# Kernel tuning notes

Measured on AMD Instinct MI355X. Metric: run time of the kernel, lower is better.

## Reference

```python
import jax, jax.numpy as jnp
import numpy as np

L, N, E = 2048, 2, 1024
H = 16
INNER = 1024
D = INNER // H  # head dim = 64
SCALE = D ** -0.5


def setup_inputs() -> dict:
    key = jax.random.key(0)
    k1, k2, k3, k4, k5 = jax.random.split(key, 5)
    return {
        "query": jax.random.normal(k1, (L, N, E), dtype=jnp.float32),
        "qkv_proj": jax.random.normal(k2, (3 * INNER, E), dtype=jnp.float32) * 0.02,
        "qkv_bias": jax.random.normal(k3, (3 * INNER,), dtype=jnp.float32) * 0.02,
        "out_proj": jax.random.normal(k4, (E, INNER), dtype=jnp.float32) * 0.02,
        "out_bias": jax.random.normal(k5, (E,), dtype=jnp.float32) * 0.02,
    }


def reference(query, qkv_proj, qkv_bias, out_proj, out_bias):
    # qkv combined projection: [L, N, 3*inner]
    qkv = jnp.einsum('lne,fe->lnf', query, qkv_proj) + qkv_bias
    # torch code views [L, N, 3*inner] as [L, N, inner, 3]: q/k/v interleaved
    qkv = qkv.reshape(L, N, INNER, 3)
    q, k, v = qkv[..., 0], qkv[..., 1], qkv[..., 2]  # each [L, N, inner]
    # [L, N*H, D] -> [N*H, L, D] (batched over batch*heads)
    q = q.reshape(L, N * H, D).transpose(1, 0, 2)
    k = k.reshape(L, N * H, D).transpose(1, 0, 2)
    v = v.reshape(L, N * H, D).transpose(1, 0, 2)
    # scores [N*H, L, L], scaled
    attn = SCALE * jnp.einsum('bld,bmd->blm', q, k)
    attn = jax.nn.softmax(attn, axis=-1)  # dropout_p = 0.0
    out = jnp.einsum('blm,bmd->bld', attn, v)  # [N*H, L, D]
    out = out.transpose(1, 0, 2).reshape(L, N, INNER)
    # output projection + bias
    return jnp.einsum('lni,ei->lne', out, out_proj) + out_bias
```

## Files before the change

### kernel.cpp

```cpp
#include <hip/hip_runtime.h>
#include <stdint.h>

#define SCALE 0.125f
#define LOG2E 1.44269504088896340736f
#define QK_SCALE (SCALE * LOG2E)

typedef __bf16 bf16x8 __attribute__((ext_vector_type(8)));
typedef float f32x4 __attribute__((ext_vector_type(4)));
typedef float f32x16 __attribute__((ext_vector_type(16)));
typedef unsigned u32x4 __attribute__((ext_vector_type(4)));

__device__ __forceinline__ ushort f2bf(float x) {
    union { float f; unsigned u; } v; v.f = x;
    unsigned r = v.u + 0x7FFFu + ((v.u >> 16) & 1u);
    return (ushort)(r >> 16);
}

__device__ __forceinline__ void gld_lds16(const void* g, void* l) {
    __builtin_amdgcn_global_load_lds(
        reinterpret_cast<const unsigned __attribute__((address_space(1)))*>(
            reinterpret_cast<uintptr_t>(g)),
        reinterpret_cast<unsigned __attribute__((address_space(3)))*>(
            (unsigned)reinterpret_cast<uintptr_t>(l)),
        16, 0, 0);
}

__global__ __launch_bounds__(256) void cast_fused(const float* __restrict__ s0,
                                                  const float* __restrict__ s1,
                                                  const float* __restrict__ s2,
                                                  ushort* __restrict__ d0,
                                                  ushort* __restrict__ d1,
                                                  ushort* __restrict__ d2) {
    int i = blockIdx.x * 256 + threadIdx.x;
    const float* src; ushort* dst; int idx;
    if (i < 1048576)            { src = s0; dst = d0; idx = i; }
    else if (i < 1048576 + 786432) { src = s1; dst = d1; idx = i - 1048576; }
    else                        { src = s2; dst = d2; idx = i - (1048576 + 786432); }
    float4 v = ((const float4*)src)[idx];
    ushort4 o;
    o.x = f2bf(v.x); o.y = f2bf(v.y); o.z = f2bf(v.z); o.w = f2bf(v.w);
    ((ushort4*)dst)[idx] = o;
}

__global__ __launch_bounds__(256, 3) void gemm_qkv(
    const ushort* __restrict__ A, const ushort* __restrict__ B,
    const float* __restrict__ bias,
    ushort* __restrict__ qh, ushort* __restrict__ kh, ushort* __restrict__ vT)
{
    __shared__ ushort As[128][64];
    __shared__ ushort Bs[128][64];
    const int tid = threadIdx.x;
    const int lane = tid & 63, wave = tid >> 6;
    const int wr = (wave >> 1) * 64, wc = (wave & 1) * 64;
    const int lr = lane & 15, lg = lane >> 4;
    const int swz = (lr & 7) << 4;
    const int sl = lane >> 3;
    const int scol = ((lane & 7) ^ sl) * 8;
    const int rowBase = blockIdx.y * 128;
    const int which = blockIdx.x >> 3;
    const int i0 = (blockIdx.x & 7) * 128;

    f32x4 acc[4][4] = {};
    for (int k0 = 0; k0 < 1024; k0 += 64) {
        __syncthreads();
        int s0 = wave * 4;
#pragma unroll
        for (int i = 0; i < 4; ++i) {
            int s = s0 + i;
            int r = s * 8 + sl;
            gld_lds16(A + (size_t)(rowBase + r) * 1024 + k0 + scol, &As[s * 8][0]);
            gld_lds16(B + (size_t)(3 * (i0 + r) + which) * 1024 + k0 + scol, &Bs[s * 8][0]);
        }
        __syncthreads();
#pragma unroll
        for (int kk = 0; kk < 2; ++kk) {
            bf16x8 af[4], bfr[4];
#pragma unroll
            for (int m = 0; m < 4; ++m)
                af[m] = *(const bf16x8*)((const char*)As + (wr + m * 16 + lr) * 128 + ((kk * 64 + lg * 16) ^ swz));
#pragma unroll
            for (int n = 0; n < 4; ++n)
                bfr[n] = *(const bf16x8*)((const char*)Bs + (wc + n * 16 + lr) * 128 + ((kk * 64 + lg * 16) ^ swz));
#pragma unroll
            for (int m = 0; m < 4; ++m)
#pragma unroll
                for (int n = 0; n < 4; ++n)
                    acc[m][n] = __builtin_amdgcn_mfma_f32_16x16x32_bf16(af[m], bfr[n], acc[m][n], 0, 0, 0);
        }
    }
#pragma unroll
    for (int n = 0; n < 4; ++n) {
        int i = i0 + wc + n * 16 + lr;
        float bv = bias[3 * i + which];
        int h = i >> 6, d = i & 63;
#pragma unroll
        for (int m = 0; m < 4; ++m) {
#pragma unroll
            for (int j = 0; j < 4; ++j) {
                int row = rowBase + wr + m * 16 + lg * 4 + j;
                int l = row >> 1, nb = row & 1;
                int bh = nb * 16 + h;
                float v = acc[m][n][j] + bv;
                if (which == 0)      qh[((size_t)bh * 2048 + l) * 64 + d] = f2bf(v * QK_SCALE);
                else if (which == 1) kh[((size_t)bh * 2048 + l) * 64 + d] = f2bf(v);
                else {
                    int lp = (l & ~12) | ((l & 4) << 1) | ((l & 8) >> 1);
                    vT[((size_t)bh * 64 + d) * 2048 + lp] = f2bf(v);
                }
            }
        }
    }
}

__global__ __launch_bounds__(256, 4) void attn_kernel(
    const ushort* __restrict__ qh, const ushort* __restrict__ kh,
    const ushort* __restrict__ vT, ushort* __restrict__ attn_out)
{
    __shared__ ushort Ks[2][64][64];
    __shared__ ushort Vs[2][64][64];
    const int tid = threadIdx.x, lane = tid & 63, wave = tid >> 6;
    const int l31 = lane & 31, hi = lane >> 5;
    const int swz = (lane & 7) << 4;
    const int b = blockIdx.y;
    const int qBase = blockIdx.x * 128;
    const int qrow = qBase + wave * 32 + l31;
    const int sl = lane >> 3;
    const int scol = ((lane & 7) ^ sl) * 8;
    const size_t kBase = (size_t)b * 2048;
    const size_t vBase = (size_t)b * 64;

    bf16x8 qf[4];
#pragma unroll
    for (int kk = 0; kk < 4; ++kk)
        qf[kk] = *(const bf16x8*)(qh + (kBase + qrow) * 64 + kk * 16 + hi * 8);

    f32x16 ot[2] = {};
    float mrun = -1e30f, lsum = 0.f;

    {
        int s0 = wave * 2;
#pragma unroll
        for (int i = 0; i < 2; ++i) {
            int s = s0 + i;
            gld_lds16(kh + (kBase + s * 8 + sl) * 64 + scol, &Ks[0][s * 8][0]);
            gld_lds16(vT + (vBase + s * 8 + sl) * 2048 + scol, &Vs[0][s * 8][0]);
        }
    }
    __syncthreads();

    int buf = 0;
    for (int t = 0; t < 32; ++t) {
        if (t < 31) {
            int s0 = wave * 2;
#pragma unroll
            for (int i = 0; i < 2; ++i) {
                int s = s0 + i;
                gld_lds16(kh + (kBase + (t + 1) * 64 + s * 8 + sl) * 64 + scol, &Ks[buf ^ 1][s * 8][0]);
                gld_lds16(vT + (vBase + s * 8 + sl) * 2048 + (t + 1) * 64 + scol, &Vs[buf ^ 1][s * 8][0]);
            }
        }
        const char* kb = (const char*)Ks + buf * 8192;
        const char* vb = (const char*)Vs + buf * 8192;

        f32x16 sc[2] = {};
        __builtin_amdgcn_s_setprio(1);
#pragma unroll
        for (int blk = 0; blk < 2; ++blk) {
#pragma unroll
            for (int kk = 0; kk < 4; ++kk) {
                bf16x8 kf = *(const bf16x8*)(kb + (blk * 32 + l31) * 128 + ((kk * 32 + hi * 16) ^ swz));
                sc[blk] = __builtin_amdgcn_mfma_f32_32x32x16_bf16(kf, qf[kk], sc[blk], 0, 0, 0);
            }
        }
        __builtin_amdgcn_s_setprio(0);

        float tm[8];
#pragma unroll
        for (int i = 0; i < 8; ++i)
            tm[i] = fmaxf(fmaxf(sc[0][i], sc[0][i + 8]), fmaxf(sc[1][i], sc[1][i + 8]));
#pragma unroll
        for (int i = 0; i < 4; ++i)
            tm[i] = fmaxf(tm[i], tm[i + 4]);
        float mx = fmaxf(fmaxf(tm[0], tm[2]), fmaxf(tm[1], tm[3]));
        mx = fmaxf(mx, __shfl_xor(mx, 32));
        if (!__all(mx - mrun <= 8.0f)) {
            float mnew = fmaxf(mrun, mx);
            float alpha = __builtin_amdgcn_exp2f(mrun - mnew);
            mrun = mnew;
            lsum *= alpha;
#pragma unroll
            for (int blk = 0; blk < 2; ++blk)
#pragma unroll
                for (int r = 0; r < 16; ++r)
                    ot[blk][r] *= alpha;
        }
#pragma unroll
        for (int blk = 0; blk < 2; ++blk)
#pragma unroll
            for (int r = 0; r < 16; ++r)
                sc[blk][r] = __builtin_amdgcn_exp2f(sc[blk][r] - mrun);
        float ts[8];
#pragma unroll
        for (int i = 0; i < 8; ++i)
            ts[i] = (sc[0][i] + sc[0][i + 8]) + (sc[1][i] + sc[1][i + 8]);
#pragma unroll
        for (int i = 0; i < 4; ++i)
            ts[i] += ts[i + 4];
        float rs = (ts[0] + ts[2]) + (ts[1] + ts[3]);
        rs += __shfl_xor(rs, 32);
        lsum += rs;

        __builtin_amdgcn_s_setprio(1);
#pragma unroll
        for (int g = 0; g < 4; ++g) {
            const int blk = g >> 1;
            const int base = (g & 1) * 8;
            unsigned A0, A1, B0, B1;
            asm("v_cvt_pk_bf16_f32 %0, %1, %2" : "=v"(A0) : "v"(sc[blk][base + 0]), "v"(sc[blk][base + 1]));
            asm("v_cvt_pk_bf16_f32 %0, %1, %2" : "=v"(A1) : "v"(sc[blk][base + 2]), "v"(sc[blk][base + 3]));
            asm("v_cvt_pk_bf16_f32 %0, %1, %2" : "=v"(B0) : "v"(sc[blk][base + 4]), "v"(sc[blk][base + 5]));
            asm("v_cvt_pk_bf16_f32 %0, %1, %2" : "=v"(B1) : "v"(sc[blk][base + 6]), "v"(sc[blk][base + 7]));
            u32x4 pw; pw[0] = A0; pw[1] = A1; pw[2] = B0; pw[3] = B1;
            bf16x8 pb = __builtin_bit_cast(bf16x8, pw);
#pragma unroll
            for (int dblk = 0; dblk < 2; ++dblk) {
                bf16x8 vf = *(const bf16x8*)(vb + (dblk * 32 + l31) * 128 + ((g * 32 + hi * 16) ^ swz));
                ot[dblk] = __builtin_amdgcn_mfma_f32_32x32x16_bf16(vf, pb, ot[dblk], 0, 0, 0);
            }
        }
        __builtin_amdgcn_s_setprio(0);
        __syncthreads();
        buf ^= 1;
    }

    const int nb = b >> 4, h = b & 15;
    float inv = __builtin_amdgcn_rcpf(lsum);
    const size_t row = (size_t)qrow * 2 + nb;
#pragma unroll
    for (int dblk = 0; dblk < 2; ++dblk) {
#pragma unroll
        for (int m = 0; m < 4; ++m) {
            float a0 = ot[dblk][4 * m + 0] * inv, a1 = ot[dblk][4 * m + 1] * inv;
            float a2 = ot[dblk][4 * m + 2] * inv, a3 = ot[dblk][4 * m + 3] * inv;
            unsigned w0, w1;
            asm("v_cvt_pk_bf16_f32 %0, %1, %2" : "=v"(w0) : "v"(a0), "v"(a1));
            asm("v_cvt_pk_bf16_f32 %0, %1, %2" : "=v"(w1) : "v"(a2), "v"(a3));
            uint2 st; st.x = w0; st.y = w1;
            *(uint2*)(attn_out + row * 1024 + h * 64 + dblk * 32 + m * 8 + hi * 4) = st;
        }
    }
}

__global__ __launch_bounds__(256, 3) void gemm_out(
    const ushort* __restrict__ A, const ushort* __restrict__ B,
    const float* __restrict__ bias, float* __restrict__ out)
{
    __shared__ ushort As[128][64];
    __shared__ ushort Bs[128][64];
    const int tid = threadIdx.x;
    const int lane = tid & 63, wave = tid >> 6;
    const int wr = (wave >> 1) * 64, wc = (wave & 1) * 64;
    const int lr = lane & 15, lg = lane >> 4;
    const int swz = (lr & 7) << 4;
    const int sl = lane >> 3;
    const int scol = ((lane & 7) ^ sl) * 8;
    const int rowBase = blockIdx.y * 128, colBase = blockIdx.x * 128;

    f32x4 acc[4][4] = {};
    for (int k0 = 0; k0 < 1024; k0 += 64) {
        __syncthreads();
        int s0 = wave * 4;
#pragma unroll
        for (int i = 0; i < 4; ++i) {
            int s = s0 + i;
            gld_lds16(A + (size_t)(rowBase + s * 8 + sl) * 1024 + k0 + scol, &As[s * 8][0]);
            gld_lds16(B + (size_t)(colBase + s * 8 + sl) * 1024 + k0 + scol, &Bs[s * 8][0]);
        }
        __syncthreads();
#pragma unroll
        for (int kk = 0; kk < 2; ++kk) {
            bf16x8 af[4], bfr[4];
#pragma unroll
            for (int m = 0; m < 4; ++m)
                af[m] = *(const bf16x8*)((const char*)As + (wr + m * 16 + lr) * 128 + ((kk * 64 + lg * 16) ^ swz));
#pragma unroll
            for (int n = 0; n < 4; ++n)
                bfr[n] = *(const bf16x8*)((const char*)Bs + (wc + n * 16 + lr) * 128 + ((kk * 64 + lg * 16) ^ swz));
#pragma unroll
            for (int m = 0; m < 4; ++m)
#pragma unroll
                for (int n = 0; n < 4; ++n)
                    acc[m][n] = __builtin_amdgcn_mfma_f32_16x16x32_bf16(af[m], bfr[n], acc[m][n], 0, 0, 0);
        }
    }
#pragma unroll
    for (int n = 0; n < 4; ++n) {
        int e = colBase + wc + n * 16 + lr;
        float bv = bias[e];
#pragma unroll
        for (int m = 0; m < 4; ++m) {
#pragma unroll
            for (int j = 0; j < 4; ++j) {
                int row = rowBase + wr + m * 16 + lg * 4 + j;
                out[(size_t)row * 1024 + e] = acc[m][n][j] + bv;
            }
        }
    }
}

extern "C" void kernel_launch(void* const* d_in, const int* in_sizes, int n_in,
                              void* d_out, int out_size, void* d_ws, size_t ws_size,
                              hipStream_t stream) {
    const float* query    = (const float*)d_in[0];
    const float* qkv_proj = (const float*)d_in[1];
    const float* qkv_bias = (const float*)d_in[2];
    const float* out_proj = (const float*)d_in[3];
    const float* out_bias = (const float*)d_in[4];
    float* out = (float*)d_out;

    char* ws = (char*)d_ws;
    ushort* qbf      = (ushort*)ws;
    ushort* wqkv     = (ushort*)(ws + (8ull << 20));
    ushort* wout     = (ushort*)(ws + (14ull << 20));
    ushort* qh       = (ushort*)(ws + (16ull << 20));
    ushort* kh       = (ushort*)(ws + (24ull << 20));
    ushort* vT       = (ushort*)(ws + (32ull << 20));
    ushort* attn_out = (ushort*)(ws + (40ull << 20));

    cast_fused<<<8192, 256, 0, stream>>>(query, qkv_proj, out_proj, qbf, wqkv, wout);
    gemm_qkv<<<dim3(24, 32), 256, 0, stream>>>(qbf, wqkv, qkv_bias, qh, kh, vT);
    attn_kernel<<<dim3(16, 32), 256, 0, stream>>>(qh, kh, vT, attn_out);
    gemm_out<<<dim3(8, 32), 256, 0, stream>>>(attn_out, wout, out_bias, out);
}
```

Before: 128.8 us.

## Split attention KV loop across two wave groups and shrink out-proj GEMM tile

The attention kernel now runs 512 threads per block. Two groups of four waves each process half of the key/value sequence with their own double-buffered LDS tiles, then merge their softmax partial results (max, sum, output) through shared memory before the final normalization and store. This doubles the waves per block and halves the serial KV loop per wave, to improve latency hiding and occupancy on the long attention loop, at the cost of 64KB of LDS and a merge step. Separately, the output-projection GEMM uses a 128x64 tile instead of 128x128, doubling the grid to 512 blocks so more CUs are filled.

New measurement: 120.2 us. 1.07x faster.

```diff
diff --git a/kernel.cpp b/kernel.cpp
--- a/kernel.cpp
+++ b/kernel.cpp
@@ -112,22 +112,25 @@
     }
 }
 
-__global__ __launch_bounds__(256, 4) void attn_kernel(
+__global__ __launch_bounds__(512, 4) void attn_kernel(
     const ushort* __restrict__ qh, const ushort* __restrict__ kh,
     const ushort* __restrict__ vT, ushort* __restrict__ attn_out)
 {
-    __shared__ ushort Ks[2][64][64];
-    __shared__ ushort Vs[2][64][64];
+    __shared__ __align__(16) char smem[65536];
     const int tid = threadIdx.x, lane = tid & 63, wave = tid >> 6;
+    const int group = wave >> 2, sub = wave & 3;
     const int l31 = lane & 31, hi = lane >> 5;
     const int swz = (lane & 7) << 4;
     const int b = blockIdx.y;
     const int qBase = blockIdx.x * 128;
-    const int qrow = qBase + wave * 32 + l31;
+    const int qrow = qBase + sub * 32 + l31;
     const int sl = lane >> 3;
     const int scol = ((lane & 7) ^ sl) * 8;
     const size_t kBase = (size_t)b * 2048;
     const size_t vBase = (size_t)b * 64;
+    char* Kg = smem + group * 16384;
+    char* Vg = smem + 32768 + group * 16384;
+    const int tg0 = group * 16;
 
     bf16x8 qf[4];
 #pragma unroll
@@ -138,29 +141,31 @@
     float mrun = -1e30f, lsum = 0.f;
 
     {
-        int s0 = wave * 2;
+        int s0 = sub * 2;
 #pragma unroll
         for (int i = 0; i < 2; ++i) {
             int s = s0 + i;
-            gld_lds16(kh + (kBase + s * 8 + sl) * 64 + scol, &Ks[0][s * 8][0]);
-            gld_lds16(vT + (vBase + s * 8 + sl) * 2048 + scol, &Vs[0][s * 8][0]);
+            gld_lds16(kh + (kBase + tg0 * 64 + s * 8 + sl) * 64 + scol, Kg + s * 1024);
+            gld_lds16(vT + (vBase + s * 8 + sl) * 2048 + tg0 * 64 + scol, Vg + s * 1024);
         }
     }
     __syncthreads();
 
     int buf = 0;
-    for (int t = 0; t < 32; ++t) {
-        if (t < 31) {
-            int s0 = wave * 2;
+    for (int t = 0; t < 16; ++t) {
+        if (t < 15) {
+            int s0 = sub * 2;
 #pragma unroll
             for (int i = 0; i < 2; ++i) {
                 int s = s0 + i;
-                gld_lds16(kh + (kBase + (t + 1) * 64 + s * 8 + sl) * 64 + scol, &Ks[buf ^ 1][s * 8][0]);
-                gld_lds16(vT + (vBase + s * 8 + sl) * 2048 + (t + 1) * 64 + scol, &Vs[buf ^ 1][s * 8][0]);
-            }
-        }
-        const char* kb = (const char*)Ks + buf * 8192;
-        const char* vb = (const char*)Vs + buf * 8192;
+                gld_lds16(kh + (kBase + (tg0 + t + 1) * 64 + s * 8 + sl) * 64 + scol,
+                          Kg + (buf ^ 1) * 8192 + s * 1024);
+                gld_lds16(vT + (vBase + s * 8 + sl) * 2048 + (tg0 + t + 1) * 64 + scol,
+                          Vg + (buf ^ 1) * 8192 + s * 1024);
+            }
+        }
+        const char* kb = Kg + buf * 8192;
+        const char* vb = Vg + buf * 8192;
 
         f32x16 sc[2] = {};
         __builtin_amdgcn_s_setprio(1);
@@ -233,20 +238,50 @@
         buf ^= 1;
     }
 
-    const int nb = b >> 4, h = b & 15;
-    float inv = __builtin_amdgcn_rcpf(lsum);
-    const size_t row = (size_t)qrow * 2 + nb;
-#pragma unroll
-    for (int dblk = 0; dblk < 2; ++dblk) {
-#pragma unroll
-        for (int m = 0; m < 4; ++m) {
-            float a0 = ot[dblk][4 * m + 0] * inv, a1 = ot[dblk][4 * m + 1] * inv;
-            float a2 = ot[dblk][4 * m + 2] * inv, a3 = ot[dblk][4 * m + 3] * inv;
-            unsigned w0, w1;
-            asm("v_cvt_pk_bf16_f32 %0, %1, %2" : "=v"(w0) : "v"(a0), "v"(a1));
-            asm("v_cvt_pk_bf16_f32 %0, %1, %2" : "=v"(w1) : "v"(a2), "v"(a3));
-            uint2 st; st.x = w0; st.y = w1;
-            *(uint2*)(attn_out + row * 1024 + h * 64 + dblk * 32 + m * 8 + hi * 4) = st;
+    float* MO = (float*)smem;
+    float* ML = (float*)(smem + 34816);
+    if (group) {
+        float* mo = MO + (sub * 32 + l31) * 68;
+#pragma unroll
+        for (int dblk = 0; dblk < 2; ++dblk)
+#pragma unroll
+            for (int m = 0; m < 4; ++m) {
+                float4 st;
+                st.x = ot[dblk][4 * m + 0]; st.y = ot[dblk][4 * m + 1];
+                st.z = ot[dblk][4 * m + 2]; st.w = ot[dblk][4 * m + 3];
+                *(float4*)(mo + dblk * 32 + m * 8 + hi * 4) = st;
+            }
+        if (!hi) {
+            ML[(sub * 32 + l31) * 2 + 0] = mrun;
+            ML[(sub * 32 + l31) * 2 + 1] = lsum;
+        }
+    }
+    __syncthreads();
+    if (!group) {
+        float m1 = ML[(sub * 32 + l31) * 2 + 0];
+        float l1 = ML[(sub * 32 + l31) * 2 + 1];
+        float mmax = fmaxf(mrun, m1);
+        float w0 = __builtin_amdgcn_exp2f(mrun - mmax);
+        float w1 = __builtin_amdgcn_exp2f(m1 - mmax);
+        float inv = __builtin_amdgcn_rcpf(lsum * w0 + l1 * w1);
+        const float* mo = MO + (sub * 32 + l31) * 68;
+        const int nb = b >> 4, h = b & 15;
+        const size_t row = (size_t)qrow * 2 + nb;
+#pragma unroll
+        for (int dblk = 0; dblk < 2; ++dblk) {
+#pragma unroll
+            for (int m = 0; m < 4; ++m) {
+                float4 oo = *(const float4*)(mo + dblk * 32 + m * 8 + hi * 4);
+                float a0 = (ot[dblk][4 * m + 0] * w0 + oo.x * w1) * inv;
+                float a1 = (ot[dblk][4 * m + 1] * w0 + oo.y * w1) * inv;
+                float a2 = (ot[dblk][4 * m + 2] * w0 + oo.z * w1) * inv;
+                float a3 = (ot[dblk][4 * m + 3] * w0 + oo.w * w1) * inv;
+                unsigned w0p, w1p;
+                asm("v_cvt_pk_bf16_f32 %0, %1, %2" : "=v"(w0p) : "v"(a0), "v"(a1));
+                asm("v_cvt_pk_bf16_f32 %0, %1, %2" : "=v"(w1p) : "v"(a2), "v"(a3));
+                uint2 st; st.x = w0p; st.y = w1p;
+                *(uint2*)(attn_out + row * 1024 + h * 64 + dblk * 32 + m * 8 + hi * 4) = st;
+            }
         }
     }
 }
@@ -256,45 +291,46 @@
     const float* __restrict__ bias, float* __restrict__ out)
 {
     __shared__ ushort As[128][64];
-    __shared__ ushort Bs[128][64];
+    __shared__ ushort Bs[64][64];
     const int tid = threadIdx.x;
     const int lane = tid & 63, wave = tid >> 6;
-    const int wr = (wave >> 1) * 64, wc = (wave & 1) * 64;
+    const int wr = (wave >> 1) * 64, wc = (wave & 1) * 32;
     const int lr = lane & 15, lg = lane >> 4;
     const int swz = (lr & 7) << 4;
     const int sl = lane >> 3;
     const int scol = ((lane & 7) ^ sl) * 8;
-    const int rowBase = blockIdx.y * 128, colBase = blockIdx.x * 128;
-
-    f32x4 acc[4][4] = {};
+    const int rowBase = blockIdx.y * 128, colBase = blockIdx.x * 64;
+
+    f32x4 acc[4][2] = {};
     for (int k0 = 0; k0 < 1024; k0 += 64) {
         __syncthreads();
-        int s0 = wave * 4;
-#pragma unroll
-        for (int i = 0; i < 4; ++i) {
-            int s = s0 + i;
-            gld_lds16(A + (size_t)(rowBase + s * 8 + sl) * 1024 + k0 + scol, &As[s * 8][0]);
-            gld_lds16(B + (size_t)(colBase + s * 8 + sl) * 1024 + k0 + scol, &Bs[s * 8][0]);
+#pragma unroll
+        for (int i = 0; i < 6; ++i) {
+            int s = wave * 6 + i;
+            if (s < 16)
+                gld_lds16(A + (size_t)(rowBase + s * 8 + sl) * 1024 + k0 + scol, &As[s * 8][0]);
+            else
+                gld_lds16(B + (size_t)(colBase + (s - 16) * 8 + sl) * 1024 + k0 + scol, &Bs[(s - 16) * 8][0]);
         }
         __syncthreads();
 #pragma unroll
         for (int kk = 0; kk < 2; ++kk) {
-            bf16x8 af[4], bfr[4];
+            bf16x8 af[4], bfr[2];
 #pragma unroll
             for (int m = 0; m < 4; ++m)
                 af[m] = *(const bf16x8*)((const char*)As + (wr + m * 16 + lr) * 128 + ((kk * 64 + lg * 16) ^ swz));
 #pragma unroll
-            for (int n = 0; n < 4; ++n)
+            for (int n = 0; n < 2; ++n)
                 bfr[n] = *(const bf16x8*)((const char*)Bs + (wc + n * 16 + lr) * 128 + ((kk * 64 + lg * 16) ^ swz));
 #pragma unroll
             for (int m = 0; m < 4; ++m)
 #pragma unroll
-                for (int n = 0; n < 4; ++n)
+                for (int n = 0; n < 2; ++n)
                     acc[m][n] = __builtin_amdgcn_mfma_f32_16x16x32_bf16(af[m], bfr[n], acc[m][n], 0, 0, 0);
         }
     }
 #pragma unroll
-    for (int n = 0; n < 4; ++n) {
+    for (int n = 0; n < 2; ++n) {
         int e = colBase + wc + n * 16 + lr;
         float bv = bias[e];
 #pragma unroll
@@ -329,6 +365,6 @@
 
     cast_fused<<<8192, 256, 0, stream>>>(query, qkv_proj, out_proj, qbf, wqkv, wout);
     gemm_qkv<<<dim3(24, 32), 256, 0, stream>>>(qbf, wqkv, qkv_bias, qh, kh, vT);
-    attn_kernel<<<dim3(16, 32), 256, 0, stream>>>(qh, kh, vT, attn_out);
-    gemm_out<<<dim3(8, 32), 256, 0, stream>>>(attn_out, wout, out_bias, out);
-}
+    attn_kernel<<<dim3(16, 32), 512, 0, stream>>>(qh, kh, vT, attn_out);
+    gemm_out<<<dim3(16, 32), 256, 0, stream>>>(attn_out, wout, out_bias, out);
+}
```
